# Kernel tuning notes

Measured on AMD Instinct MI355X. Metric: run time of the kernel, lower is better.

Reference implementation:

```python
import jax, jax.numpy as jnp
import numpy as np

N_NODES = 100000
N_EDGES = 600000
H = 128


def setup_inputs() -> dict:
    key = jax.random.key(0)
    k_z, k_e, k_w1, k_w2 = jax.random.split(key, 4)
    z = jax.random.normal(k_z, (N_NODES, H), dtype=jnp.float32)
    edge_index = jax.random.randint(k_e, (2, N_EDGES), 0, N_NODES, dtype=jnp.int64)
    # Kaiming-ish init scale for the MLP weights
    W1 = jax.random.normal(k_w1, (2 * H, H), dtype=jnp.float32) * (1.0 / np.sqrt(2 * H))
    b1 = jnp.zeros((H,), dtype=jnp.float32)
    W2 = jax.random.normal(k_w2, (H, 1), dtype=jnp.float32) * (1.0 / np.sqrt(H))
    b2 = jnp.zeros((1,), dtype=jnp.float32)
    return {"z": z, "edge_index": edge_index, "W1": W1, "b1": b1, "W2": W2, "b2": b2}


def reference(z, edge_index, W1, b1, W2, b2):
    # Gather source/destination node embeddings: [E, H] each
    src = z[edge_index[0]]
    dst = z[edge_index[1]]
    # Avoid materializing the [E, 2H] concat: split W1 into src/dst blocks
    # so fc1(cat(src,dst)) == src @ W1[:H] + dst @ W1[H:] + b1
    h = src @ W1[:H] + dst @ W1[H:] + b1  # [E, H]
    h = jax.nn.relu(h)
    out = h @ W2 + b2  # [E, 1]
    return out.reshape(-1)
```

## Files before the change

### kernel.cpp

```cpp
#include <hip/hip_runtime.h>
#include <hip/hip_bf16.h>
#include <stdint.h>

#define N_NODES_C 100000
#define N_EDGES_C 600000
#define H_C 128

typedef __bf16 bf16x8 __attribute__((ext_vector_type(8)));
typedef float f32x16 __attribute__((ext_vector_type(16)));
typedef float f32x4v __attribute__((ext_vector_type(4)));
typedef _Float16 half8 __attribute__((ext_vector_type(8)));
typedef unsigned short ushort8 __attribute__((ext_vector_type(8)));

#define LDS_STRIDE 136

__device__ __forceinline__ unsigned short f2bf(float f) {
    unsigned int u = __builtin_bit_cast(unsigned int, f);
    u += 0x7fffu + ((u >> 16) & 1u);
    return (unsigned short)(u >> 16);
}

__global__ void w1fmt_kernel(const float* __restrict__ W1,
                             unsigned short* __restrict__ w1f) {
    int i = blockIdx.x * blockDim.x + threadIdx.x;
    if (i >= 8 * 8 * 64 * 8) return;
    int j = i & 7;
    int L = (i >> 3) & 63;
    int t = (i >> 9) & 7;
    int s = (i >> 12) & 7;
    int k  = s * 16 + ((L >> 5) * 8) + j;
    int n2 = t * 32 + (L & 31);
    float w = (n2 < 128) ? W1[k * H_C + n2]
                         : W1[(128 + k) * H_C + (n2 - 128)];
    w1f[i] = f2bf(w);
}

__launch_bounds__(256, 2)
__global__ void node_gemm_kernel(const float* __restrict__ z,
                                 const unsigned short* __restrict__ w1f,
                                 const float* __restrict__ b1,
                                 _Float16* __restrict__ uv) {
    __shared__ unsigned short smem[32 * LDS_STRIDE];

    const int lane = threadIdx.x & 63;
    const int wv   = threadIdx.x >> 6;
    const int l31  = lane & 31;
    const int half = lane >> 5;
    const int uh   = wv >> 1;
    const int tile = blockIdx.x;

    {
        const int sr = threadIdx.x >> 3;
        const int sc = (threadIdx.x & 7) * 16;
        const float* src = z + (size_t)(tile * 32 + sr) * H_C + sc;
        f32x4v f0 = *reinterpret_cast<const f32x4v*>(src);
        f32x4v f1 = *reinterpret_cast<const f32x4v*>(src + 4);
        f32x4v f2 = *reinterpret_cast<const f32x4v*>(src + 8);
        f32x4v f3 = *reinterpret_cast<const f32x4v*>(src + 12);
        ushort8 lo, hi;
        #pragma unroll
        for (int j = 0; j < 4; ++j) {
            lo[j]     = f2bf(f0[j]);
            lo[j + 4] = f2bf(f1[j]);
            hi[j]     = f2bf(f2[j]);
            hi[j + 4] = f2bf(f3[j]);
        }
        *reinterpret_cast<ushort8*>(smem + sr * LDS_STRIDE + sc)     = lo;
        *reinterpret_cast<ushort8*>(smem + sr * LDS_STRIDE + sc + 8) = hi;
    }

    bf16x8 bfrag[8][2];
    #pragma unroll
    for (int s = 0; s < 8; ++s) {
        #pragma unroll
        for (int t = 0; t < 2; ++t) {
            bfrag[s][t] = reinterpret_cast<const bf16x8*>(w1f)
                              [(s * 8 + wv * 2 + t) * 64 + lane];
        }
    }

    float badd[2];
    int   ncol[2];
    #pragma unroll
    for (int t = 0; t < 2; ++t) {
        int n2  = (wv * 2 + t) * 32 + l31;
        ncol[t] = n2 - uh * 128;
        badd[t] = uh ? 0.0f : b1[n2];
    }
    const size_t segbase = uh ? (size_t)N_NODES_C * H_C : 0;

    __syncthreads();

    f32x16 acc[2] = {};
    #pragma unroll
    for (int s = 0; s < 8; ++s) {
        bf16x8 a = *reinterpret_cast<const bf16x8*>(
                       smem + l31 * LDS_STRIDE + s * 16 + half * 8);
        acc[0] = __builtin_amdgcn_mfma_f32_32x32x16_bf16(a, bfrag[s][0], acc[0], 0, 0, 0);
        acc[1] = __builtin_amdgcn_mfma_f32_32x32x16_bf16(a, bfrag[s][1], acc[1], 0, 0, 0);
    }

    const int node0 = tile * 32;
    #pragma unroll
    for (int t = 0; t < 2; ++t) {
        #pragma unroll
        for (int r = 0; r < 16; ++r) {
            int row = (r & 3) + 8 * (r >> 2) + 4 * half;
            float v = acc[t][r] + badd[t];
            float fo = __shfl_xor(v, 1);
            if ((lane & 1) == 0) {
                unsigned int pk = __builtin_bit_cast(
                    unsigned int, __builtin_amdgcn_cvt_pkrtz(v, fo));
                size_t idx = segbase + (size_t)(node0 + row) * H_C + ncol[t];
                *reinterpret_cast<unsigned int*>(uv + idx) = pk;
            }
        }
    }
}

__global__ void edge_kernel(const _Float16* __restrict__ uv,
                            const int* __restrict__ ei,
                            const float* __restrict__ w2,
                            const float* __restrict__ b2,
                            float* __restrict__ out) {
    const int tid = blockIdx.x * blockDim.x + threadIdx.x;
    const int j   = tid & 15;
    const int q   = tid >> 4;
    const int e0  = q * 8;
    if (e0 >= N_EDGES_C) return;

    float w2v[8];
    {
        f32x4v a = *reinterpret_cast<const f32x4v*>(w2 + j * 8);
        f32x4v b = *reinterpret_cast<const f32x4v*>(w2 + j * 8 + 4);
        #pragma unroll
        for (int k = 0; k < 4; ++k) { w2v[k] = a[k]; w2v[k + 4] = b[k]; }
    }
    const float c2 = b2[0];
    const _Float16* vbase = uv + (size_t)N_NODES_C * H_C;

    int4 sa = *reinterpret_cast<const int4*>(ei + e0);
    int4 sb = *reinterpret_cast<const int4*>(ei + e0 + 4);
    int4 da = *reinterpret_cast<const int4*>(ei + N_EDGES_C + e0);
    int4 db = *reinterpret_cast<const int4*>(ei + N_EDGES_C + e0 + 4);

    int se[8] = { sa.x, sa.y, sa.z, sa.w, sb.x, sb.y, sb.z, sb.w };
    int de[8] = { da.x, da.y, da.z, da.w, db.x, db.y, db.z, db.w };

    half8 uu[8], vv[8];
    #pragma unroll
    for (int i = 0; i < 8; ++i) {
        uu[i] = *reinterpret_cast<const half8*>(uv    + (size_t)se[i] * H_C + j * 8);
        vv[i] = *reinterpret_cast<const half8*>(vbase + (size_t)de[i] * H_C + j * 8);
    }

    float p[8];
    #pragma unroll
    for (int i = 0; i < 8; ++i) {
        float acc = 0.0f;
        #pragma unroll
        for (int k = 0; k < 8; ++k) {
            float h = (float)uu[i][k] + (float)vv[i][k];
            h = h > 0.0f ? h : 0.0f;
            acc = fmaf(h, w2v[k], acc);
        }
        p[i] = acc;
    }
    #pragma unroll
    for (int m = 1; m <= 8; m <<= 1) {
        #pragma unroll
        for (int i = 0; i < 8; ++i) p[i] += __shfl_xor(p[i], m);
    }
    if (j == 0) {
        float4 o0 = { p[0] + c2, p[1] + c2, p[2] + c2, p[3] + c2 };
        float4 o1 = { p[4] + c2, p[5] + c2, p[6] + c2, p[7] + c2 };
        *reinterpret_cast<float4*>(out + e0)     = o0;
        *reinterpret_cast<float4*>(out + e0 + 4) = o1;
    }
}

extern "C" void kernel_launch(void* const* d_in, const int* in_sizes, int n_in,
                              void* d_out, int out_size, void* d_ws, size_t ws_size,
                              hipStream_t stream) {
    const float* z  = (const float*)d_in[0];
    const int*   ei = (const int*)d_in[1];
    const float* W1 = (const float*)d_in[2];
    const float* b1 = (const float*)d_in[3];
    const float* W2 = (const float*)d_in[4];
    const float* b2 = (const float*)d_in[5];
    float* out = (float*)d_out;

    unsigned short* w1f = (unsigned short*)d_ws;
    _Float16* uv = (_Float16*)((char*)d_ws + 65536);

    w1fmt_kernel<<<(8 * 8 * 64 * 8 + 255) / 256, 256, 0, stream>>>(W1, w1f);

    node_gemm_kernel<<<N_NODES_C / 32, 256, 0, stream>>>(z, w1f, b1, uv);

    int nquarters = N_EDGES_C / 8;
    edge_kernel<<<(nquarters * 16 + 255) / 256, 256, 0, stream>>>(uv, ei, W2, b2, out);
}
```

Measured before the change: 151.2 us.

## Fuse weight formatting, node GEMM and edge pass into one persistent kernel

Replaces three kernel launches with one persistent kernel of 512 blocks. Each block converts its W1 fragment directly from fp32, loops over node tiles with a register prefetch of the next tile, then all blocks meet at a software grid barrier built on atomic flags before the grid-strided edge gather/MLP phase. This removes launch overhead and the separate W1 formatting pass. In exchange it adds a memset, a spin-wait barrier that relies on all 512 blocks being co-resident, and lower parallelism in each phase.

```diff
diff --git a/kernel.cpp b/kernel.cpp
--- a/kernel.cpp
+++ b/kernel.cpp
@@ -1,10 +1,16 @@
 #include <hip/hip_runtime.h>
-#include <hip/hip_bf16.h>
 #include <stdint.h>
 
 #define N_NODES_C 100000
 #define N_EDGES_C 600000
 #define H_C 128
+
+#define NTILES 3125
+#define NB 512
+#define TPB 512
+#define NQ 75000
+#define QSTR 16384
+#define LDS_STRIDE 136
 
 typedef __bf16 bf16x8 __attribute__((ext_vector_type(8)));
 typedef float f32x16 __attribute__((ext_vector_type(16)));
@@ -12,170 +18,177 @@
 typedef _Float16 half8 __attribute__((ext_vector_type(8)));
 typedef unsigned short ushort8 __attribute__((ext_vector_type(8)));
 
-#define LDS_STRIDE 136
-
 __device__ __forceinline__ unsigned short f2bf(float f) {
     unsigned int u = __builtin_bit_cast(unsigned int, f);
     u += 0x7fffu + ((u >> 16) & 1u);
     return (unsigned short)(u >> 16);
 }
 
-__global__ void w1fmt_kernel(const float* __restrict__ W1,
-                             unsigned short* __restrict__ w1f) {
-    int i = blockIdx.x * blockDim.x + threadIdx.x;
-    if (i >= 8 * 8 * 64 * 8) return;
-    int j = i & 7;
-    int L = (i >> 3) & 63;
-    int t = (i >> 9) & 7;
-    int s = (i >> 12) & 7;
-    int k  = s * 16 + ((L >> 5) * 8) + j;
-    int n2 = t * 32 + (L & 31);
-    float w = (n2 < 128) ? W1[k * H_C + n2]
-                         : W1[(128 + k) * H_C + (n2 - 128)];
-    w1f[i] = f2bf(w);
-}
-
-__launch_bounds__(256, 2)
-__global__ void node_gemm_kernel(const float* __restrict__ z,
-                                 const unsigned short* __restrict__ w1f,
-                                 const float* __restrict__ b1,
-                                 _Float16* __restrict__ uv) {
+__device__ __forceinline__ int agent_ld_relaxed(int* p) {
+    return __hip_atomic_load(p, __ATOMIC_RELAXED, __HIP_MEMORY_SCOPE_AGENT);
+}
+__device__ __forceinline__ void agent_st_relaxed(int* p, int v) {
+    __hip_atomic_store(p, v, __ATOMIC_RELAXED, __HIP_MEMORY_SCOPE_AGENT);
+}
+
+__launch_bounds__(TPB, 4)
+__global__ void fused_kernel(const float* __restrict__ z,
+                             const int* __restrict__ ei,
+                             const float* __restrict__ W1,
+                             const float* __restrict__ b1,
+                             const float* __restrict__ w2,
+                             const float* __restrict__ b2,
+                             float* __restrict__ out,
+                             int* __restrict__ bar,
+                             _Float16* __restrict__ uv) {
     __shared__ unsigned short smem[32 * LDS_STRIDE];
 
-    const int lane = threadIdx.x & 63;
-    const int wv   = threadIdx.x >> 6;
+    const int tid  = threadIdx.x;
+    const int bid  = blockIdx.x;
+    const int lane = tid & 63;
+    const int wv   = tid >> 6;
     const int l31  = lane & 31;
     const int half = lane >> 5;
-    const int uh   = wv >> 1;
-    const int tile = blockIdx.x;
-
+    const int uh   = wv >> 2;
+    const int ncol = (wv & 3) * 32 + l31;
+
+    bf16x8 bfrag[8];
     {
-        const int sr = threadIdx.x >> 3;
-        const int sc = (threadIdx.x & 7) * 16;
-        const float* src = z + (size_t)(tile * 32 + sr) * H_C + sc;
-        f32x4v f0 = *reinterpret_cast<const f32x4v*>(src);
-        f32x4v f1 = *reinterpret_cast<const f32x4v*>(src + 4);
-        f32x4v f2 = *reinterpret_cast<const f32x4v*>(src + 8);
-        f32x4v f3 = *reinterpret_cast<const f32x4v*>(src + 12);
-        ushort8 lo, hi;
-        #pragma unroll
-        for (int j = 0; j < 4; ++j) {
-            lo[j]     = f2bf(f0[j]);
-            lo[j + 4] = f2bf(f1[j]);
-            hi[j]     = f2bf(f2[j]);
-            hi[j + 4] = f2bf(f3[j]);
-        }
-        *reinterpret_cast<ushort8*>(smem + sr * LDS_STRIDE + sc)     = lo;
-        *reinterpret_cast<ushort8*>(smem + sr * LDS_STRIDE + sc + 8) = hi;
-    }
-
-    bf16x8 bfrag[8][2];
-    #pragma unroll
-    for (int s = 0; s < 8; ++s) {
-        #pragma unroll
-        for (int t = 0; t < 2; ++t) {
-            bfrag[s][t] = reinterpret_cast<const bf16x8*>(w1f)
-                              [(s * 8 + wv * 2 + t) * 64 + lane];
-        }
-    }
-
-    float badd[2];
-    int   ncol[2];
-    #pragma unroll
-    for (int t = 0; t < 2; ++t) {
-        int n2  = (wv * 2 + t) * 32 + l31;
-        ncol[t] = n2 - uh * 128;
-        badd[t] = uh ? 0.0f : b1[n2];
-    }
-    const size_t segbase = uh ? (size_t)N_NODES_C * H_C : 0;
-
-    __syncthreads();
-
-    f32x16 acc[2] = {};
-    #pragma unroll
-    for (int s = 0; s < 8; ++s) {
-        bf16x8 a = *reinterpret_cast<const bf16x8*>(
-                       smem + l31 * LDS_STRIDE + s * 16 + half * 8);
-        acc[0] = __builtin_amdgcn_mfma_f32_32x32x16_bf16(a, bfrag[s][0], acc[0], 0, 0, 0);
-        acc[1] = __builtin_amdgcn_mfma_f32_32x32x16_bf16(a, bfrag[s][1], acc[1], 0, 0, 0);
-    }
-
-    const int node0 = tile * 32;
-    #pragma unroll
-    for (int t = 0; t < 2; ++t) {
+        const float* wb = W1 + (size_t)(uh * H_C + half * 8) * H_C + ncol;
+        #pragma unroll
+        for (int s = 0; s < 8; ++s) {
+            #pragma unroll
+            for (int j = 0; j < 8; ++j) {
+                unsigned short b = f2bf(wb[(s * 16 + j) * H_C]);
+                bfrag[s][j] = __builtin_bit_cast(__bf16, b);
+            }
+        }
+    }
+    const float  badd    = uh ? 0.0f : b1[wv * 32 + l31];
+    const size_t segbase = uh ? (size_t)N_NODES_C * H_C : (size_t)0;
+
+    const int sr = tid >> 4;
+    const int sc = (tid & 15) * 8;
+
+    int t = bid;
+    f32x4v fa, fb;
+    {
+        const float* src = z + (size_t)(t * 32 + sr) * H_C + sc;
+        fa = *reinterpret_cast<const f32x4v*>(src);
+        fb = *reinterpret_cast<const f32x4v*>(src + 4);
+    }
+    for (;;) {
+        __syncthreads();
+        {
+            ushort8 u8;
+            #pragma unroll
+            for (int jj = 0; jj < 4; ++jj) {
+                u8[jj]     = f2bf(fa[jj]);
+                u8[jj + 4] = f2bf(fb[jj]);
+            }
+            *reinterpret_cast<ushort8*>(smem + sr * LDS_STRIDE + sc) = u8;
+        }
+        const int tn = t + NB;
+        if (tn < NTILES) {
+            const float* src = z + (size_t)(tn * 32 + sr) * H_C + sc;
+            fa = *reinterpret_cast<const f32x4v*>(src);
+            fb = *reinterpret_cast<const f32x4v*>(src + 4);
+        }
+        __syncthreads();
+
+        f32x16 acc = {};
+        #pragma unroll
+        for (int s = 0; s < 8; ++s) {
+            bf16x8 a = *reinterpret_cast<const bf16x8*>(
+                           smem + l31 * LDS_STRIDE + s * 16 + half * 8);
+            acc = __builtin_amdgcn_mfma_f32_32x32x16_bf16(a, bfrag[s], acc, 0, 0, 0);
+        }
+
+        const int node0 = t * 32;
         #pragma unroll
         for (int r = 0; r < 16; ++r) {
-            int row = (r & 3) + 8 * (r >> 2) + 4 * half;
-            float v = acc[t][r] + badd[t];
+            const int row = (r & 3) + 8 * (r >> 2) + 4 * half;
+            float v  = acc[r] + badd;
             float fo = __shfl_xor(v, 1);
             if ((lane & 1) == 0) {
                 unsigned int pk = __builtin_bit_cast(
                     unsigned int, __builtin_amdgcn_cvt_pkrtz(v, fo));
-                size_t idx = segbase + (size_t)(node0 + row) * H_C + ncol[t];
-                *reinterpret_cast<unsigned int*>(uv + idx) = pk;
-            }
-        }
-    }
-}
-
-__global__ void edge_kernel(const _Float16* __restrict__ uv,
-                            const int* __restrict__ ei,
-                            const float* __restrict__ w2,
-                            const float* __restrict__ b2,
-                            float* __restrict__ out) {
-    const int tid = blockIdx.x * blockDim.x + threadIdx.x;
-    const int j   = tid & 15;
-    const int q   = tid >> 4;
-    const int e0  = q * 8;
-    if (e0 >= N_EDGES_C) return;
-
+                *reinterpret_cast<unsigned int*>(
+                    uv + segbase + (size_t)(node0 + row) * H_C + ncol) = pk;
+            }
+        }
+        if (tn >= NTILES) break;
+        t = tn;
+    }
+
+    __syncthreads();
+    if (tid == 0) {
+        __threadfence();
+        agent_st_relaxed(&bar[bid], 1);
+    }
+    if (bid == 0) {
+        for (int i = tid; i < NB; i += TPB)
+            while (agent_ld_relaxed(&bar[i]) == 0) {}
+        __syncthreads();
+        if (tid == 0) agent_st_relaxed(&bar[NB], 1);
+    }
+    if (tid == 0) {
+        while (agent_ld_relaxed(&bar[NB]) == 0) {}
+        __threadfence();
+    }
+    __syncthreads();
+
+    const int ql = tid & 15;
     float w2v[8];
     {
-        f32x4v a = *reinterpret_cast<const f32x4v*>(w2 + j * 8);
-        f32x4v b = *reinterpret_cast<const f32x4v*>(w2 + j * 8 + 4);
+        f32x4v a = *reinterpret_cast<const f32x4v*>(w2 + ql * 8);
+        f32x4v b = *reinterpret_cast<const f32x4v*>(w2 + ql * 8 + 4);
         #pragma unroll
         for (int k = 0; k < 4; ++k) { w2v[k] = a[k]; w2v[k + 4] = b[k]; }
     }
     const float c2 = b2[0];
-    const _Float16* vbase = uv + (size_t)N_NODES_C * H_C;
-
-    int4 sa = *reinterpret_cast<const int4*>(ei + e0);
-    int4 sb = *reinterpret_cast<const int4*>(ei + e0 + 4);
-    int4 da = *reinterpret_cast<const int4*>(ei + N_EDGES_C + e0);
-    int4 db = *reinterpret_cast<const int4*>(ei + N_EDGES_C + e0 + 4);
-
-    int se[8] = { sa.x, sa.y, sa.z, sa.w, sb.x, sb.y, sb.z, sb.w };
-    int de[8] = { da.x, da.y, da.z, da.w, db.x, db.y, db.z, db.w };
-
-    half8 uu[8], vv[8];
-    #pragma unroll
-    for (int i = 0; i < 8; ++i) {
-        uu[i] = *reinterpret_cast<const half8*>(uv    + (size_t)se[i] * H_C + j * 8);
-        vv[i] = *reinterpret_cast<const half8*>(vbase + (size_t)de[i] * H_C + j * 8);
-    }
-
-    float p[8];
-    #pragma unroll
-    for (int i = 0; i < 8; ++i) {
-        float acc = 0.0f;
-        #pragma unroll
-        for (int k = 0; k < 8; ++k) {
-            float h = (float)uu[i][k] + (float)vv[i][k];
-            h = h > 0.0f ? h : 0.0f;
-            acc = fmaf(h, w2v[k], acc);
-        }
-        p[i] = acc;
-    }
-    #pragma unroll
-    for (int m = 1; m <= 8; m <<= 1) {
-        #pragma unroll
-        for (int i = 0; i < 8; ++i) p[i] += __shfl_xor(p[i], m);
-    }
-    if (j == 0) {
-        float4 o0 = { p[0] + c2, p[1] + c2, p[2] + c2, p[3] + c2 };
-        float4 o1 = { p[4] + c2, p[5] + c2, p[6] + c2, p[7] + c2 };
-        *reinterpret_cast<float4*>(out + e0)     = o0;
-        *reinterpret_cast<float4*>(out + e0 + 4) = o1;
+    const _Float16* __restrict__ vb = uv + (size_t)N_NODES_C * H_C;
+
+    for (int q = (bid * TPB + tid) >> 4; q < NQ; q += QSTR) {
+        const int e0 = q * 8;
+        int4 sa = *reinterpret_cast<const int4*>(ei + e0);
+        int4 sb = *reinterpret_cast<const int4*>(ei + e0 + 4);
+        int4 da = *reinterpret_cast<const int4*>(ei + N_EDGES_C + e0);
+        int4 db = *reinterpret_cast<const int4*>(ei + N_EDGES_C + e0 + 4);
+
+        int se[8] = { sa.x, sa.y, sa.z, sa.w, sb.x, sb.y, sb.z, sb.w };
+        int de[8] = { da.x, da.y, da.z, da.w, db.x, db.y, db.z, db.w };
+
+        half8 uu[8], vv[8];
+        #pragma unroll
+        for (int i = 0; i < 8; ++i) {
+            uu[i] = *reinterpret_cast<const half8*>(uv + (size_t)se[i] * H_C + ql * 8);
+            vv[i] = *reinterpret_cast<const half8*>(vb + (size_t)de[i] * H_C + ql * 8);
+        }
+
+        float p[8];
+        #pragma unroll
+        for (int i = 0; i < 8; ++i) {
+            float acc = 0.0f;
+            #pragma unroll
+            for (int k = 0; k < 8; ++k) {
+                float h = (float)uu[i][k] + (float)vv[i][k];
+                h = h > 0.0f ? h : 0.0f;
+                acc = fmaf(h, w2v[k], acc);
+            }
+            p[i] = acc;
+        }
+        #pragma unroll
+        for (int m = 1; m <= 8; m <<= 1) {
+            #pragma unroll
+            for (int i = 0; i < 8; ++i) p[i] += __shfl_xor(p[i], m);
+        }
+        if (ql == 0) {
+            float4 o0 = { p[0] + c2, p[1] + c2, p[2] + c2, p[3] + c2 };
+            float4 o1 = { p[4] + c2, p[5] + c2, p[6] + c2, p[7] + c2 };
+            *reinterpret_cast<float4*>(out + e0)     = o0;
+            *reinterpret_cast<float4*>(out + e0 + 4) = o1;
+        }
     }
 }
 
@@ -190,13 +203,9 @@
     const float* b2 = (const float*)d_in[5];
     float* out = (float*)d_out;
 
-    unsigned short* w1f = (unsigned short*)d_ws;
-    _Float16* uv = (_Float16*)((char*)d_ws + 65536);
-
-    w1fmt_kernel<<<(8 * 8 * 64 * 8 + 255) / 256, 256, 0, stream>>>(W1, w1f);
-
-    node_gemm_kernel<<<N_NODES_C / 32, 256, 0, stream>>>(z, w1f, b1, uv);
-
-    int nquarters = N_EDGES_C / 8;
-    edge_kernel<<<(nquarters * 16 + 255) / 256, 256, 0, stream>>>(uv, ei, W2, b2, out);
-}
+    int* bar = (int*)d_ws;
+    _Float16* uv = (_Float16*)((char*)d_ws + 4096);
+
+    hipMemsetAsync(d_ws, 0, 4096, stream);
+    fused_kernel<<<NB, TPB, 0, stream>>>(z, ei, W1, b1, W2, b2, out, bar, uv);
+}
```

After: 179.9 us. 19.0% more time.

## Process two node tiles per block with prefetched second tile

Applied to the files above, without the earlier changes.

Each node-GEMM block now handles two 32-node tiles. It loads the W1 fragments once and reuses them for both tiles. The z rows for the second tile are loaded into registers while the first tile's MFMA and store phase runs, and go into a second LDS buffer. The aim is to amortize the W1 fragment loads and hide global load latency, at the cost of more registers and LDS per block and half as many blocks.

```diff
diff --git a/kernel.cpp b/kernel.cpp
--- a/kernel.cpp
+++ b/kernel.cpp
@@ -5,6 +5,8 @@
 #define N_NODES_C 100000
 #define N_EDGES_C 600000
 #define H_C 128
+
+#define NTILES 3125
 
 typedef __bf16 bf16x8 __attribute__((ext_vector_type(8)));
 typedef float f32x16 __attribute__((ext_vector_type(16)));
@@ -40,23 +42,46 @@
                                  const unsigned short* __restrict__ w1f,
                                  const float* __restrict__ b1,
                                  _Float16* __restrict__ uv) {
-    __shared__ unsigned short smem[32 * LDS_STRIDE];
+    __shared__ unsigned short smem[2][32 * LDS_STRIDE];
 
     const int lane = threadIdx.x & 63;
     const int wv   = threadIdx.x >> 6;
     const int l31  = lane & 31;
     const int half = lane >> 5;
     const int uh   = wv >> 1;
-    const int tile = blockIdx.x;
+    const int t0   = blockIdx.x * 2;
+    const int t1   = t0 + 1;
+
+    const int sr = threadIdx.x >> 3;
+    const int sc = (threadIdx.x & 7) * 16;
+
+    const float* src0 = z + (size_t)(t0 * 32 + sr) * H_C + sc;
+    f32x4v f0 = *reinterpret_cast<const f32x4v*>(src0);
+    f32x4v f1 = *reinterpret_cast<const f32x4v*>(src0 + 4);
+    f32x4v f2 = *reinterpret_cast<const f32x4v*>(src0 + 8);
+    f32x4v f3 = *reinterpret_cast<const f32x4v*>(src0 + 12);
+
+    bf16x8 bfrag[8][2];
+    #pragma unroll
+    for (int s = 0; s < 8; ++s) {
+        #pragma unroll
+        for (int t = 0; t < 2; ++t) {
+            bfrag[s][t] = reinterpret_cast<const bf16x8*>(w1f)
+                              [(s * 8 + wv * 2 + t) * 64 + lane];
+        }
+    }
+
+    float badd[2];
+    int   ncol[2];
+    #pragma unroll
+    for (int t = 0; t < 2; ++t) {
+        int n2  = (wv * 2 + t) * 32 + l31;
+        ncol[t] = n2 - uh * 128;
+        badd[t] = uh ? 0.0f : b1[n2];
+    }
+    const size_t segbase = uh ? (size_t)N_NODES_C * H_C : 0;
 
     {
-        const int sr = threadIdx.x >> 3;
-        const int sc = (threadIdx.x & 7) * 16;
-        const float* src = z + (size_t)(tile * 32 + sr) * H_C + sc;
-        f32x4v f0 = *reinterpret_cast<const f32x4v*>(src);
-        f32x4v f1 = *reinterpret_cast<const f32x4v*>(src + 4);
-        f32x4v f2 = *reinterpret_cast<const f32x4v*>(src + 8);
-        f32x4v f3 = *reinterpret_cast<const f32x4v*>(src + 12);
         ushort8 lo, hi;
         #pragma unroll
         for (int j = 0; j < 4; ++j) {
@@ -65,54 +90,86 @@
             hi[j]     = f2bf(f2[j]);
             hi[j + 4] = f2bf(f3[j]);
         }
-        *reinterpret_cast<ushort8*>(smem + sr * LDS_STRIDE + sc)     = lo;
-        *reinterpret_cast<ushort8*>(smem + sr * LDS_STRIDE + sc + 8) = hi;
-    }
-
-    bf16x8 bfrag[8][2];
-    #pragma unroll
-    for (int s = 0; s < 8; ++s) {
+        *reinterpret_cast<ushort8*>(smem[0] + sr * LDS_STRIDE + sc)     = lo;
+        *reinterpret_cast<ushort8*>(smem[0] + sr * LDS_STRIDE + sc + 8) = hi;
+    }
+
+    f32x4v g0, g1, g2, g3;
+    if (t1 < NTILES) {
+        const float* src1 = z + (size_t)(t1 * 32 + sr) * H_C + sc;
+        g0 = *reinterpret_cast<const f32x4v*>(src1);
+        g1 = *reinterpret_cast<const f32x4v*>(src1 + 4);
+        g2 = *reinterpret_cast<const f32x4v*>(src1 + 8);
+        g3 = *reinterpret_cast<const f32x4v*>(src1 + 12);
+    }
+
+    __syncthreads();
+
+    {
+        f32x16 acc[2] = {};
+        #pragma unroll
+        for (int s = 0; s < 8; ++s) {
+            bf16x8 a = *reinterpret_cast<const bf16x8*>(
+                           smem[0] + l31 * LDS_STRIDE + s * 16 + half * 8);
+            acc[0] = __builtin_amdgcn_mfma_f32_32x32x16_bf16(a, bfrag[s][0], acc[0], 0, 0, 0);
+            acc[1] = __builtin_amdgcn_mfma_f32_32x32x16_bf16(a, bfrag[s][1], acc[1], 0, 0, 0);
+        }
+        const int node0 = t0 * 32;
         #pragma unroll
         for (int t = 0; t < 2; ++t) {
-            bfrag[s][t] = reinterpret_cast<const bf16x8*>(w1f)
-                              [(s * 8 + wv * 2 + t) * 64 + lane];
-        }
-    }
-
-    float badd[2];
-    int   ncol[2];
-    #pragma unroll
-    for (int t = 0; t < 2; ++t) {
-        int n2  = (wv * 2 + t) * 32 + l31;
-        ncol[t] = n2 - uh * 128;
-        badd[t] = uh ? 0.0f : b1[n2];
-    }
-    const size_t segbase = uh ? (size_t)N_NODES_C * H_C : 0;
+            #pragma unroll
+            for (int r = 0; r < 16; ++r) {
+                int row = (r & 3) + 8 * (r >> 2) + 4 * half;
+                float v = acc[t][r] + badd[t];
+                float fo = __shfl_xor(v, 1);
+                if ((lane & 1) == 0) {
+                    unsigned int pk = __builtin_bit_cast(
+                        unsigned int, __builtin_amdgcn_cvt_pkrtz(v, fo));
+                    size_t idx = segbase + (size_t)(node0 + row) * H_C + ncol[t];
+                    *reinterpret_cast<unsigned int*>(uv + idx) = pk;
+                }
+            }
+        }
+    }
+
+    if (t1 < NTILES) {
+        ushort8 lo, hi;
+        #pragma unroll
+        for (int j = 0; j < 4; ++j) {
+            lo[j]     = f2bf(g0[j]);
+            lo[j + 4] = f2bf(g1[j]);
+            hi[j]     = f2bf(g2[j]);
+            hi[j + 4] = f2bf(g3[j]);
+        }
+        *reinterpret_cast<ushort8*>(smem[1] + sr * LDS_STRIDE + sc)     = lo;
+        *reinterpret_cast<ushort8*>(smem[1] + sr * LDS_STRIDE + sc + 8) = hi;
+    }
 
     __syncthreads();
 
-    f32x16 acc[2] = {};
-    #pragma unroll
-    for (int s = 0; s < 8; ++s) {
-        bf16x8 a = *reinterpret_cast<const bf16x8*>(
-                       smem + l31 * LDS_STRIDE + s * 16 + half * 8);
-        acc[0] = __builtin_amdgcn_mfma_f32_32x32x16_bf16(a, bfrag[s][0], acc[0], 0, 0, 0);
-        acc[1] = __builtin_amdgcn_mfma_f32_32x32x16_bf16(a, bfrag[s][1], acc[1], 0, 0, 0);
-    }
-
-    const int node0 = tile * 32;
-    #pragma unroll
-    for (int t = 0; t < 2; ++t) {
-        #pragma unroll
-        for (int r = 0; r < 16; ++r) {
-            int row = (r & 3) + 8 * (r >> 2) + 4 * half;
-            float v = acc[t][r] + badd[t];
-            float fo = __shfl_xor(v, 1);
-            if ((lane & 1) == 0) {
-                unsigned int pk = __builtin_bit_cast(
-                    unsigned int, __builtin_amdgcn_cvt_pkrtz(v, fo));
-                size_t idx = segbase + (size_t)(node0 + row) * H_C + ncol[t];
-                *reinterpret_cast<unsigned int*>(uv + idx) = pk;
+    if (t1 < NTILES) {
+        f32x16 acc[2] = {};
+        #pragma unroll
+        for (int s = 0; s < 8; ++s) {
+            bf16x8 a = *reinterpret_cast<const bf16x8*>(
+                           smem[1] + l31 * LDS_STRIDE + s * 16 + half * 8);
+            acc[0] = __builtin_amdgcn_mfma_f32_32x32x16_bf16(a, bfrag[s][0], acc[0], 0, 0, 0);
+            acc[1] = __builtin_amdgcn_mfma_f32_32x32x16_bf16(a, bfrag[s][1], acc[1], 0, 0, 0);
+        }
+        const int node0 = t1 * 32;
+        #pragma unroll
+        for (int t = 0; t < 2; ++t) {
+            #pragma unroll
+            for (int r = 0; r < 16; ++r) {
+                int row = (r & 3) + 8 * (r >> 2) + 4 * half;
+                float v = acc[t][r] + badd[t];
+                float fo = __shfl_xor(v, 1);
+                if ((lane & 1) == 0) {
+                    unsigned int pk = __builtin_bit_cast(
+                        unsigned int, __builtin_amdgcn_cvt_pkrtz(v, fo));
+                    size_t idx = segbase + (size_t)(node0 + row) * H_C + ncol[t];
+                    *reinterpret_cast<unsigned int*>(uv + idx) = pk;
+                }
             }
         }
     }
@@ -195,7 +252,7 @@
 
     w1fmt_kernel<<<(8 * 8 * 64 * 8 + 255) / 256, 256, 0, stream>>>(W1, w1f);
 
-    node_gemm_kernel<<<N_NODES_C / 32, 256, 0, stream>>>(z, w1f, b1, uv);
+    node_gemm_kernel<<<(NTILES + 1) / 2, 256, 0, stream>>>(z, w1f, b1, uv);
 
     int nquarters = N_EDGES_C / 8;
     edge_kernel<<<(nquarters * 16 + 255) / 256, 256, 0, stream>>>(uv, ei, W2, b2, out);
```

Result: no change. 151.5 us (+0.2%).
